# Kernel tuning notes

Measured on AMD Instinct MI355X. Metric: run time of the kernel, lower is better.

The kernel has to match this reference:

```python
import jax, jax.numpy as jnp
import numpy as np

B, SEQ, D = 4, 1024, 1024
H = 16
HD = D // H            # 64, matches cos/sin last dim
S_COLS, TOPK = 8, 2
INTER = 768            # find_multiple(round(1.0 * D * 2 / 3), 256)
EPS = 1e-5


def setup_inputs() -> dict:
    key = jax.random.key(0)
    ks = jax.random.split(key, 6)
    hidden_states = jax.random.normal(ks[0], (B, SEQ, D), jnp.float32)
    # RoPE tables (standard rotary, theta=10000)
    inv_freq = 1.0 / (10000.0 ** (jnp.arange(0, HD, 2, dtype=jnp.float32) / HD))
    freqs = jnp.outer(jnp.arange(SEQ, dtype=jnp.float32), inv_freq)
    emb = jnp.concatenate([freqs, freqs], axis=-1)  # [SEQ, HD]
    cos, sin = jnp.cos(emb), jnp.sin(emb)
    Wr = jax.random.normal(ks[1], (S_COLS, D), jnp.float32) * 0.02
    temperature = jnp.ones((1,), jnp.float32)
    # Stacked per-column TransformerBlock params (bias-free linears)
    Wqkv = jax.random.normal(ks[2], (S_COLS, D, 3 * D), jnp.float32) * 0.02
    Wo = jax.random.normal(ks[3], (S_COLS, D, D), jnp.float32) * 0.02
    Wgu = jax.random.normal(ks[4], (S_COLS, D, 2 * INTER), jnp.float32) * 0.02
    Wd = jax.random.normal(ks[5], (S_COLS, INTER, D), jnp.float32) * 0.02
    return dict(hidden_states=hidden_states, cos=cos, sin=sin, Wr=Wr,
                temperature=temperature, Wqkv=Wqkv, Wo=Wo, Wgu=Wgu, Wd=Wd)


def _rms_norm(x):
    return x * jax.lax.rsqrt(jnp.mean(x * x, axis=-1, keepdims=True) + EPS)


def _rotate_half(x):
    x1, x2 = jnp.split(x, 2, axis=-1)
    return jnp.concatenate([-x2, x1], axis=-1)


def _columns_forward(x, Wqkv, Wo, Wgu, Wd, cos, sin):
    # x: [n, seq, D] dispatched sequences; params gathered per dispatch entry [n, ...]
    n, seq, d = x.shape
    qkv = jnp.einsum('nsd,nde->nse', x, Wqkv)
    q, k, v = jnp.split(qkv, 3, axis=-1)
    q = q.reshape(n, seq, H, HD)
    k = k.reshape(n, seq, H, HD)
    v = v.reshape(n, seq, H, HD)
    c = cos[None, :, None, :]
    s = sin[None, :, None, :]
    q = q * c + _rotate_half(q) * s
    k = k * c + _rotate_half(k) * s
    scores = jnp.einsum('nqhd,nkhd->nhqk', q, k) / jnp.sqrt(jnp.asarray(HD, x.dtype))
    attn = jax.nn.softmax(scores, axis=-1)  # non-causal (HRM-style block)
    ctx = jnp.einsum('nhqk,nkhd->nqhd', attn, v).reshape(n, seq, d)
    attn_out = jnp.einsum('nsd,nde->nse', ctx, Wo)
    x = _rms_norm(x + attn_out)                      # post-norm residual
    gu = jnp.einsum('nsd,nde->nse', x, Wgu)
    gate, up = jnp.split(gu, 2, axis=-1)
    mlp_out = jnp.einsum('nsi,nid->nsd', jax.nn.silu(gate) * up, Wd)
    return _rms_norm(x + mlp_out)


def reference(hidden_states, cos, sin, Wr, temperature, Wqkv, Wo, Wgu, Wd):
    Bn = hidden_states.shape[0]
    temp = jnp.clip(temperature, 0.1, 10.0)
    routing_logits = (hidden_states.mean(axis=1) @ Wr.T) / temp   # [B, S]
    topk_vals, topk_idx = jax.lax.top_k(routing_logits, TOPK)
    weights = jax.nn.softmax(topk_vals, axis=-1)                  # [B, k]
    flat_idx = topk_idx.reshape(-1)                               # [B*k] expert ids
    flat_w = weights.reshape(-1)
    sample_idx = jnp.repeat(jnp.arange(Bn), TOPK)                 # [B*k]
    # Sparse dispatch: exactly B*k block forwards via per-entry param gather
    x_disp = hidden_states[sample_idx]
    col_out = _columns_forward(x_disp, Wqkv[flat_idx], Wo[flat_idx],
                               Wgu[flat_idx], Wd[flat_idx], cos, sin)
    result = jnp.zeros_like(hidden_states).at[sample_idx].add(
        flat_w[:, None, None] * col_out)
    return result, routing_logits
```

## Files before the change

kernel.cpp:

```cpp
#include <hip/hip_runtime.h>
#include <hip/hip_bf16.h>
#include <math.h>

#define B_     4
#define SEQ_   1024
#define D_     1024
#define H_     16
#define NE_    8
#define INTER_ 768
#define EPS_   1e-5f

typedef unsigned short u16;
typedef __attribute__((ext_vector_type(8))) short s8v;
typedef __attribute__((ext_vector_type(4))) short s4v;
typedef __attribute__((ext_vector_type(4))) float f4v;
typedef __attribute__((ext_vector_type(4))) unsigned short u16x4;
typedef __attribute__((ext_vector_type(8))) unsigned short u16x8;

__device__ __forceinline__ u16 f2bf(float x) {
    union { float f; unsigned u; } c; c.f = x;
    unsigned r = (c.u + 0x7FFFu + ((c.u >> 16) & 1u)) >> 16;
    return (u16)r;
}
__device__ __forceinline__ float bf2f(u16 h) {
    union { unsigned u; float f; } c; c.u = ((unsigned)h) << 16;
    return c.f;
}
__device__ __forceinline__ unsigned pk2(float a, float b) {
    union { float f; unsigned u; } x, y; x.f = a; y.f = b;
    return ((x.u + 0x8000u) >> 16) | ((y.u + 0x8000u) & 0xffff0000u);
}

#define GLDS16(gp, lp) \
    __builtin_amdgcn_global_load_lds((const __attribute__((address_space(1))) unsigned int*)(gp), \
                                     (__attribute__((address_space(3))) unsigned int*)(lp), 16, 0, 0)

#define BARRIER()  asm volatile("s_barrier" ::: "memory")

__global__ void route1(const float* __restrict__ hidden, float* __restrict__ part,
                       u16* __restrict__ hb) {
    int b = blockIdx.x, ch = blockIdx.y, t = threadIdx.x;
    const float* xb = hidden + (size_t)b * SEQ_ * D_ + (size_t)ch * 32 * D_;
    u16* ho = hb + (size_t)b * SEQ_ * D_ + (size_t)ch * 32 * D_;
    float4 acc = make_float4(0.f, 0.f, 0.f, 0.f);
    for (int r = 0; r < 32; ++r) {
        float4 v = *(const float4*)&xb[(size_t)r * D_ + t * 4];
        acc.x += v.x; acc.y += v.y; acc.z += v.z; acc.w += v.w;
        u16x4 o = {f2bf(v.x), f2bf(v.y), f2bf(v.z), f2bf(v.w)};
        *(u16x4*)&ho[(size_t)r * D_ + t * 4] = o;
    }
    *(float4*)&part[((size_t)(b * 32 + ch)) * D_ + t * 4] = acc;
}

__global__ void route2(const float* __restrict__ part, const float* __restrict__ Wr,
                       const float* __restrict__ temp, float* __restrict__ out_logits,
                       int* __restrict__ flat_idx, float* __restrict__ flat_w) {
    __shared__ float col[1024];
    __shared__ float sm[8];
    int b = blockIdx.x, t = threadIdx.x;
    float4 s = make_float4(0.f, 0.f, 0.f, 0.f);
    for (int ch = 0; ch < 32; ++ch) {
        float4 v = *(const float4*)&part[((size_t)(b * 32 + ch)) * D_ + t * 4];
        s.x += v.x; s.y += v.y; s.z += v.z; s.w += v.w;
    }
    col[t * 4 + 0] = s.x * (1.f / 1024.f);
    col[t * 4 + 1] = s.y * (1.f / 1024.f);
    col[t * 4 + 2] = s.z * (1.f / 1024.f);
    col[t * 4 + 3] = s.w * (1.f / 1024.f);
    __syncthreads();
    int j = t >> 5, d0 = t & 31;
    float p = 0.f;
    for (int d = d0; d < 1024; d += 32) p += col[d] * Wr[j * 1024 + d];
    for (int off = 16; off >= 1; off >>= 1) p += __shfl_down(p, off, 32);
    if (d0 == 0) sm[j] = p;
    __syncthreads();
    if (t == 0) {
        float tc = temp[0];
        tc = fminf(fmaxf(tc, 0.1f), 10.0f);
        float lg[8];
        for (int jj = 0; jj < 8; ++jj) {
            lg[jj] = sm[jj] / tc;
            out_logits[b * 8 + jj] = lg[jj];
        }
        int i0 = 0; float v0 = lg[0];
        for (int jj = 1; jj < 8; ++jj) if (lg[jj] > v0) { v0 = lg[jj]; i0 = jj; }
        int i1 = -1; float v1 = -1e30f;
        for (int jj = 0; jj < 8; ++jj) if (jj != i0 && lg[jj] > v1) { v1 = lg[jj]; i1 = jj; }
        float e1 = expf(v1 - v0);
        flat_idx[2 * b]     = i0;
        flat_idx[2 * b + 1] = i1;
        flat_w[2 * b]       = 1.0f / (1.0f + e1);
        flat_w[2 * b + 1]   = e1 / (1.0f + e1);
    }
}

__global__ __launch_bounds__(256) void wtrans_all(const float* __restrict__ Wqkv,
                                                  const float* __restrict__ Wo,
                                                  const float* __restrict__ Wgu,
                                                  const float* __restrict__ Wd,
                                                  u16* __restrict__ WqkvT, u16* __restrict__ WoT,
                                                  u16* __restrict__ WguT, u16* __restrict__ WdT,
                                                  const int* __restrict__ flat_idx) {
    int bid = blockIdx.x;
    const float* W; u16* Wt; int K, N, nx, gu = 0;
    if (bid < 6144)      { W = Wqkv; Wt = WqkvT; K = 1024; N = 3072; nx = 48; }
    else if (bid < 8192) { bid -= 6144;  W = Wo;  Wt = WoT;  K = 1024; N = 1024; nx = 16; }
    else if (bid < 11264){ bid -= 8192;  W = Wgu; Wt = WguT; K = 1024; N = 1536; nx = 24; gu = 1; }
    else                 { bid -= 11264; W = Wd;  Wt = WdT;  K = 768;  N = 1024; nx = 16; }
    int x = bid % nx; bid /= nx;
    int ny = K >> 6;
    int y = bid % ny;
    int e = bid / ny;

    bool used = false;
#pragma unroll
    for (int jj = 0; jj < 8; ++jj) used |= (flat_idx[jj] == e);
    if (!used) return;

    __shared__ float tile[64][65];
    int k0 = y * 64, n0 = x * 64;
    const float* Wp = W + (size_t)e * K * N;
    u16* Wtp = Wt + (size_t)e * K * N;
    int t = threadIdx.x;
    int kk = t >> 4, ns = t & 15;
#pragma unroll
    for (int p = 0; p < 4; ++p) {
        float4 v = *(const float4*)&Wp[(size_t)(k0 + kk + p * 16) * N + n0 + ns * 4];
        tile[kk + p * 16][ns * 4 + 0] = v.x;
        tile[kk + p * 16][ns * 4 + 1] = v.y;
        tile[kk + p * 16][ns * 4 + 2] = v.z;
        tile[kk + p * 16][ns * 4 + 3] = v.w;
    }
    __syncthreads();
    int nn = t >> 3, ks = t & 7;
#pragma unroll
    for (int p = 0; p < 2; ++p) {
        int n = n0 + nn + p * 32;
        int nd = n;
        if (gu) nd = (n < 768) ? ((n >> 4) << 5) + (n & 15)
                               : (((n - 768) >> 4) << 5) + 16 + (n & 15);
        u16x8 o;
#pragma unroll
        for (int jj = 0; jj < 8; ++jj) o[jj] = f2bf(tile[ks * 8 + jj][nn + p * 32]);
        *(u16x8*)&Wtp[(size_t)nd * K + k0 + ks * 8] = o;
    }
}

#define GEMM_STAGE(Ap_, Wp_, Kp_, k0v, bo)                                                  \
    {                                                                                       \
        _Pragma("unroll") for (int it = 0; it < 2; ++it) {                                  \
            int p = it * 256 + w * 64 + lane;                                               \
            int row = p >> 2, seg = (p & 3) ^ ((row >> 1) & 3);                             \
            GLDS16((Ap_) + (size_t)(m0 + row) * (Kp_) + (k0v) + seg * 8,                    \
                   As + (bo) + (size_t)(it * 256 + w * 64) * 8);                            \
            GLDS16((Wp_) + (size_t)(n0 + row) * (Kp_) + (k0v) + seg * 8,                    \
                   Bs + (bo) + (size_t)(it * 256 + w * 64) * 8);                            \
        }                                                                                   \
    }

#define GEMM_CORE(Ap_, Wp_, Kp_)                                                            \
    f4v acc[4][4];                                                                          \
    _Pragma("unroll") for (int i = 0; i < 4; ++i)                                           \
        _Pragma("unroll") for (int jj = 0; jj < 4; ++jj) acc[i][jj] = (f4v){0.f,0.f,0.f,0.f}; \
    const int NT = (Kp_) / 32;                                                              \
    GEMM_STAGE(Ap_, Wp_, Kp_, 0, 0)                                                         \
    GEMM_STAGE(Ap_, Wp_, Kp_, 32, 4096)                                                     \
    GEMM_STAGE(Ap_, Wp_, Kp_, 64, 8192)                                                     \
    asm volatile("s_waitcnt vmcnt(8)" ::: "memory");                                        \
    BARRIER();                                                                              \
    int cb = 0;                                                                             \
    for (int kt = 0; kt < NT; ++kt) {                                                       \
        int bo = cb * 4096;                                                                 \
        s8v af[4], bfr[4];                                                                  \
        _Pragma("unroll") for (int ti = 0; ti < 4; ++ti) {                                  \
            int r = wm + ti * 16 + c;                                                       \
            af[ti]  = *(const s8v*)&As[bo + r * 32 + (g ^ ((r >> 1) & 3)) * 8];             \
        }                                                                                   \
        _Pragma("unroll") for (int tj = 0; tj < 4; ++tj) {                                  \
            int r = wn + tj * 16 + c;                                                       \
            bfr[tj] = *(const s8v*)&Bs[bo + r * 32 + (g ^ ((r >> 1) & 3)) * 8];             \
        }                                                                                   \
        __builtin_amdgcn_s_setprio(1);                                                      \
        _Pragma("unroll") for (int ti = 0; ti < 4; ++ti)                                    \
            _Pragma("unroll") for (int tj = 0; tj < 4; ++tj)                                \
                acc[ti][tj] = __builtin_amdgcn_mfma_f32_16x16x32_bf16(af[ti], bfr[tj], acc[ti][tj], 0, 0, 0); \
        __builtin_amdgcn_s_setprio(0);                                                      \
        BARRIER();                                                                          \
        if (kt + 3 < NT) {                                                                  \
            GEMM_STAGE(Ap_, Wp_, Kp_, (kt + 3) * 32, bo)                                    \
            asm volatile("s_waitcnt vmcnt(8)" ::: "memory");                                \
        } else if (kt + 2 < NT) {                                                           \
            asm volatile("s_waitcnt vmcnt(4)" ::: "memory");                                \
        } else {                                                                            \
            asm volatile("s_waitcnt vmcnt(0)" ::: "memory");                                \
        }                                                                                   \
        BARRIER();                                                                          \
        cb = (cb == 2) ? 0 : cb + 1;                                                        \
    }

__global__ __launch_bounds__(256) void gemm_bf16(const u16* __restrict__ Abase,
                                                 const u16* __restrict__ Wtbase,
                                                 u16* __restrict__ Cb,
                                                 const int* __restrict__ flat_idx,
                                                 int M, int N, int K, int aDiv) {
    __shared__ __align__(16) u16 As[3 * 128 * 32];
    __shared__ __align__(16) u16 Bs[3 * 128 * 32];
    int e = blockIdx.z;
    const u16* A  = Abase + (size_t)(e / aDiv) * M * K;
    const u16* Wt = Wtbase + (size_t)flat_idx[e] * N * K;
    int m0 = blockIdx.y * 128, n0 = blockIdx.x * 128;
    int t = threadIdx.x, lane = t & 63, w = t >> 6;
    int g = lane >> 4, c = lane & 15;
    int wm = (w >> 1) * 64, wn = (w & 1) * 64;

    GEMM_CORE(A, Wt, K)

    u16* C = Cb + (size_t)e * M * N;
#pragma unroll
    for (int ti = 0; ti < 4; ++ti)
#pragma unroll
        for (int tj = 0; tj < 4; ++tj)
#pragma unroll
            for (int i = 0; i < 4; ++i)
                C[(size_t)(m0 + wm + ti * 16 + g * 4 + i) * N + n0 + wn + tj * 16 + c] = f2bf(acc[ti][tj][i]);
}

__global__ __launch_bounds__(256) void gemm_qkv(const u16* __restrict__ Abase,
                                                const u16* __restrict__ Wtbase,
                                                const int* __restrict__ flat_idx,
                                                const float* __restrict__ cosb,
                                                const float* __restrict__ sinb,
                                                u16* __restrict__ Qb, u16* __restrict__ Kb,
                                                u16* __restrict__ Vb) {
    __shared__ __align__(16) u16 As[3 * 128 * 32];
    __shared__ __align__(16) u16 Bs[3 * 128 * 32];
    const int K = 1024, N = 3072;
    int e = blockIdx.z;
    const u16* A  = Abase + (size_t)(e >> 1) * 1024 * K;
    const u16* Wt = Wtbase + (size_t)flat_idx[e] * N * K;
    int m0 = blockIdx.y * 128, n0 = blockIdx.x * 128;
    int t = threadIdx.x, lane = t & 63, w = t >> 6;
    int g = lane >> 4, c = lane & 15;
    int wm = (w >> 1) * 64, wn = (w & 1) * 64;

    GEMM_CORE(A, Wt, K)

    int col0 = n0 + wn;
    int sb = m0 + wm + g * 4;
    if (col0 < 2048) {
        bool isq = col0 < 1024;
        u16* dst = isq ? Qb : Kb;
        int h = (col0 & 1023) >> 6;
        const float scl = isq ? 0.125f * 1.44269504f : 1.0f;
#pragma unroll
        for (int ti = 0; ti < 4; ++ti)
#pragma unroll
            for (int i = 0; i < 4; ++i) {
                int s = sb + ti * 16 + i;
                size_t ob = ((size_t)(e * 1024) + s) * 1024 + h * 64;
#pragma unroll
                for (int tj = 0; tj < 2; ++tj) {
                    int d = tj * 16 + c;
                    float x1 = acc[ti][tj][i], x2 = acc[ti][tj + 2][i];
                    float c1 = cosb[s * 64 + d],      s1 = sinb[s * 64 + d];
                    float c2 = cosb[s * 64 + d + 32], s2 = sinb[s * 64 + d + 32];
                    dst[ob + d]      = f2bf((x1 * c1 - x2 * s1) * scl);
                    dst[ob + d + 32] = f2bf((x2 * c2 + x1 * s2) * scl);
                }
            }
    } else {
        int vcol = col0 - 2048;
#pragma unroll
        for (int ti = 0; ti < 4; ++ti)
#pragma unroll
            for (int tj = 0; tj < 4; ++tj)
#pragma unroll
                for (int i = 0; i < 4; ++i)
                    Vb[((size_t)(e * 1024) + sb + ti * 16 + i) * 1024 + vcol + tj * 16 + c] = f2bf(acc[ti][tj][i]);
    }
}

__global__ __launch_bounds__(256) void gemm_wgu_silu(const u16* __restrict__ Abase,
                                                     const u16* __restrict__ Wtbase,
                                                     u16* __restrict__ act,
                                                     const int* __restrict__ flat_idx) {
    __shared__ __align__(16) u16 As[3 * 128 * 32];
    __shared__ __align__(16) u16 Bs[3 * 128 * 32];
    const int K = 1024, N = 1536;
    int e = blockIdx.z;
    const u16* A  = Abase + (size_t)e * 1024 * K;
    const u16* Wt = Wtbase + (size_t)flat_idx[e] * N * K;
    int m0 = blockIdx.y * 128, n0 = blockIdx.x * 128;
    int t = threadIdx.x, lane = t & 63, w = t >> 6;
    int g = lane >> 4, c = lane & 15;
    int wm = (w >> 1) * 64, wn = (w & 1) * 64;

    GEMM_CORE(A, Wt, K)

    int col0 = n0 + wn;
    int oc0 = (col0 >> 1) + c;
    int sb = m0 + wm + g * 4;
#pragma unroll
    for (int ti = 0; ti < 4; ++ti)
#pragma unroll
        for (int i = 0; i < 4; ++i) {
            size_t rb = ((size_t)(e * 1024) + sb + ti * 16 + i) * 768;
#pragma unroll
            for (int pr = 0; pr < 2; ++pr) {
                float gt = acc[ti][pr * 2][i];
                float up = acc[ti][pr * 2 + 1][i];
                act[rb + oc0 + pr * 16] = f2bf(gt / (1.f + __expf(-gt)) * up);
            }
        }
}

__global__ __launch_bounds__(256) void vtrans(const u16* __restrict__ Vb, u16* __restrict__ Vtg) {
    __shared__ __align__(16) u16 tile[64 * 72];
    int s0 = blockIdx.x * 64;
    int eh = blockIdx.y;
    int e = eh >> 4, h = eh & 15;
    int t = threadIdx.x;
#pragma unroll
    for (int it = 0; it < 2; ++it) {
        int p = it * 256 + t;
        int sr = p >> 3, ds = p & 7;
        u16x8 v = *(const u16x8*)&Vb[((size_t)(e * 1024) + s0 + sr) * 1024 + h * 64 + ds * 8];
        *(u16x8*)&tile[sr * 72 + ds * 8] = v;
    }
    __syncthreads();
#pragma unroll
    for (int it = 0; it < 2; ++it) {
        int p = it * 256 + t;
        int d = p >> 3, ks = p & 7;
        u16x8 o;
#pragma unroll
        for (int jj = 0; jj < 8; ++jj) o[jj] = tile[(ks * 8 + jj) * 72 + d];
        *(u16x8*)&Vtg[((size_t)((e * 16 + h) * 64) + d) * 1024 + s0 + ks * 8] = o;
    }
}

#define ATTN_STAGE(ktv, bo)                                                                 \
    {                                                                                       \
        _Pragma("unroll") for (int it = 0; it < 2; ++it) {                                  \
            int p = it * 256 + w * 64 + lane;                                               \
            int row = p >> 3, ss = p & 7;                                                   \
            GLDS16(Kb + ((size_t)(e * 1024 + (ktv) * 64 + row)) * 1024 + h * 64 + (ss ^ (row & 7)) * 8, \
                   Ks + (bo) + (size_t)(it * 256 + w * 64) * 8);                            \
            GLDS16(Vtg + ((size_t)((e * 16 + h) * 64 + row)) * 1024 + (ktv) * 64 + (ss ^ (row & 7)) * 8, \
                   Vt + (bo) + (size_t)(it * 256 + w * 64) * 8);                            \
        }                                                                                   \
    }

__global__ __launch_bounds__(256) void attn_mfma(const u16* __restrict__ Qb, const u16* __restrict__ Kb,
                                                 const u16* __restrict__ Vtg, u16* __restrict__ ctx) {
    __shared__ __align__(16) u16 Ks[2 * 64 * 64];
    __shared__ __align__(16) u16 Vt[2 * 64 * 64];
    int e = blockIdx.x, h = blockIdx.y, qt = blockIdx.z;
    int t = threadIdx.x, lane = t & 63, w = t >> 6;
    int g = lane >> 4, c = lane & 15;
    int q0 = qt * 64 + w * 16;

    s8v qf[2];
#pragma unroll
    for (int ks = 0; ks < 2; ++ks)
        qf[ks] = *(const s8v*)&Qb[((size_t)(e * 1024) + q0 + c) * 1024 + h * 64 + ks * 32 + g * 8];

    f4v O[4];
#pragma unroll
    for (int tj = 0; tj < 4; ++tj) O[tj] = (f4v){0.f, 0.f, 0.f, 0.f};
    f4v liacc = (f4v){0.f, 0.f, 0.f, 0.f};
    const s4v vone = {(short)0x3F80, (short)0x3F80, (short)0x3F80, (short)0x3F80};

    ATTN_STAGE(0, 0)
    ATTN_STAGE(1, 4096)
    asm volatile("s_waitcnt vmcnt(4)" ::: "memory");
    BARRIER();
    int cb = 0;

    for (int kt = 0; kt < 16; ++kt) {
        int bo = cb * 4096;
        f4v st[4];
#pragma unroll
        for (int tj = 0; tj < 4; ++tj) st[tj] = (f4v){0.f, 0.f, 0.f, 0.f};
#pragma unroll
        for (int ks = 0; ks < 2; ++ks)
#pragma unroll
            for (int tj = 0; tj < 4; ++tj) {
                int kvl = tj * 16 + c;
                s8v kf = *(const s8v*)&Ks[bo + kvl * 64 + (((ks * 4 + g) ^ (kvl & 7)) * 8)];
                st[tj] = __builtin_amdgcn_mfma_f32_16x16x32_bf16(kf, qf[ks], st[tj], 0, 0, 0);
            }

        s4v pf[4];
#pragma unroll
        for (int tj = 0; tj < 4; ++tj) {
            float p0 = __builtin_amdgcn_exp2f(st[tj][0]);
            float p1 = __builtin_amdgcn_exp2f(st[tj][1]);
            float p2 = __builtin_amdgcn_exp2f(st[tj][2]);
            float p3 = __builtin_amdgcn_exp2f(st[tj][3]);
            union { unsigned u[2]; s4v v; } pu;
            pu.u[0] = pk2(p0, p1);
            pu.u[1] = pk2(p2, p3);
            pf[tj] = pu.v;
        }

#pragma unroll
        for (int tjC = 0; tjC < 4; ++tjC) {
            liacc = __builtin_amdgcn_mfma_f32_16x16x16bf16_1k(pf[tjC], vone, liacc, 0, 0, 0);
#pragma unroll
            for (int tjd = 0; tjd < 4; ++tjd) {
                int d = tjd * 16 + c;
                int sd = tjC * 2 + (g >> 1);
                s4v vf = *(const s4v*)&Vt[bo + d * 64 + ((sd ^ (d & 7)) * 8) + (g & 1) * 4];
                O[tjd] = __builtin_amdgcn_mfma_f32_16x16x16bf16_1k(pf[tjC], vf, O[tjd], 0, 0, 0);
            }
        }

        BARRIER();
        if (kt + 2 < 16) {
            ATTN_STAGE(kt + 2, bo)
            asm volatile("s_waitcnt vmcnt(4)" ::: "memory");
        } else {
            asm volatile("s_waitcnt vmcnt(0)" ::: "memory");
        }
        BARRIER();
        cb ^= 1;
    }
#pragma unroll
    for (int i = 0; i < 4; ++i) {
        float linv = 1.0f / liacc[i];
        size_t rbase = ((size_t)(e * 1024) + q0 + g * 4 + i) * 1024 + h * 64;
#pragma unroll
        for (int tjd = 0; tjd < 4; ++tjd)
            ctx[rbase + tjd * 16 + c] = f2bf(O[tjd][i] * linv);
    }
}

__global__ void add_rmsnorm(const u16* __restrict__ hb, const u16* __restrict__ aob,
                            u16* __restrict__ xnb) {
    int row = blockIdx.x;
    int e = row >> 10;
    int b = e >> 1;
    int s = row & 1023;
    const u16* xr = hb + (((size_t)b * SEQ_ + s) << 10);
    const u16* ar = aob + ((size_t)row << 10);
    u16* o = xnb + ((size_t)row << 10);
    int t = threadIdx.x;
    u16x4 xv = *(const u16x4*)&xr[t * 4];
    u16x4 av = *(const u16x4*)&ar[t * 4];
    float v[4];
    float ss = 0.f;
#pragma unroll
    for (int i = 0; i < 4; ++i) {
        v[i] = bf2f(xv[i]) + bf2f(av[i]);
        ss += v[i] * v[i];
    }
    for (int off = 32; off >= 1; off >>= 1) ss += __shfl_down(ss, off, 64);
    __shared__ float wred[4];
    if ((t & 63) == 0) wred[t >> 6] = ss;
    __syncthreads();
    float tot = wred[0] + wred[1] + wred[2] + wred[3];
    float scale = rsqrtf(tot * (1.0f / 1024.0f) + EPS_);
    u16x4 ov;
#pragma unroll
    for (int i = 0; i < 4; ++i) ov[i] = f2bf(v[i] * scale);
    *(u16x4*)&o[t * 4] = ov;
}

__global__ void final_kernel(const u16* __restrict__ xnb, const u16* __restrict__ mlpb,
                             const float* __restrict__ flat_w, float* __restrict__ out) {
    int row = blockIdx.x;
    int b = row >> 10;
    int s = row & 1023;
    int t = threadIdx.x;
    __shared__ float wred[4];
    float res[4] = {0.f, 0.f, 0.f, 0.f};
    for (int j = 0; j < 2; ++j) {
        int e = 2 * b + j;
        size_t off = (((size_t)e * SEQ_ + s) << 10);
        u16x4 xv = *(const u16x4*)&xnb[off + t * 4];
        u16x4 mv = *(const u16x4*)&mlpb[off + t * 4];
        float v[4];
        float ss = 0.f;
#pragma unroll
        for (int i = 0; i < 4; ++i) {
            v[i] = bf2f(xv[i]) + bf2f(mv[i]);
            ss += v[i] * v[i];
        }
        for (int off2 = 32; off2 >= 1; off2 >>= 1) ss += __shfl_down(ss, off2, 64);
        if ((t & 63) == 0) wred[t >> 6] = ss;
        __syncthreads();
        float tot = wred[0] + wred[1] + wred[2] + wred[3];
        float scale = rsqrtf(tot * (1.0f / 1024.0f) + EPS_);
        float wgt = flat_w[e];
#pragma unroll
        for (int i = 0; i < 4; ++i) res[i] += wgt * v[i] * scale;
        __syncthreads();
    }
    float* o = out + ((size_t)row << 10);
    *(float4*)&o[t * 4] = make_float4(res[0], res[1], res[2], res[3]);
}

extern "C" void kernel_launch(void* const* d_in, const int* in_sizes, int n_in,
                              void* d_out, int out_size, void* d_ws, size_t ws_size,
                              hipStream_t stream) {
    const float* hidden = (const float*)d_in[0];
    const float* cosb   = (const float*)d_in[1];
    const float* sinb   = (const float*)d_in[2];
    const float* Wr     = (const float*)d_in[3];
    const float* temp   = (const float*)d_in[4];
    const float* Wqkv   = (const float*)d_in[5];
    const float* Wo     = (const float*)d_in[6];
    const float* Wgu    = (const float*)d_in[7];
    const float* Wd     = (const float*)d_in[8];
    float* out = (float*)d_out;
    float* out_logits = out + (size_t)B_ * SEQ_ * D_;

    char* base = (char*)d_ws;
    int*   flat_idx = (int*)base;
    float* flat_w   = (float*)(base + 128);
    float* routeP   = (float*)(base + 4096);
    size_t off = (size_t)1 << 20;
    u16* WqkvT = (u16*)(base + off); off += (size_t)8 * 3072 * 1024 * 2;
    u16* WoT   = (u16*)(base + off); off += (size_t)8 * 1024 * 1024 * 2;
    u16* WguT  = (u16*)(base + off); off += (size_t)8 * 1536 * 1024 * 2;
    u16* WdT   = (u16*)(base + off); off += (size_t)8 * 1024 * 768 * 2;
    u16* hb    = (u16*)(base + off); off += (size_t)4 * 1024 * 1024 * 2;
    u16* Qb    = (u16*)(base + off); off += (size_t)8 * 1024 * 1024 * 2;
    u16* Kb    = (u16*)(base + off); off += (size_t)8 * 1024 * 1024 * 2;
    u16* Vb    = (u16*)(base + off); off += (size_t)8 * 1024 * 1024 * 2;
    u16* Vtg   = (u16*)(base + off); off += (size_t)8 * 1024 * 1024 * 2;
    u16* ctxb  = (u16*)(base + off); off += (size_t)8 * 1024 * 1024 * 2;
    u16* aob   = (u16*)(base + off); off += (size_t)8 * 1024 * 1024 * 2;
    u16* xnb   = (u16*)(base + off); off += (size_t)8 * 1024 * 1024 * 2;
    u16* actb  = (u16*)(base + off); off += (size_t)8 * 1024 * 768 * 2;
    u16* mlpb  = (u16*)(base + off); off += (size_t)8 * 1024 * 1024 * 2;

    route1<<<dim3(4, 32), 256, 0, stream>>>(hidden, routeP, hb);
    route2<<<4, 256, 0, stream>>>(routeP, Wr, temp, out_logits, flat_idx, flat_w);
    wtrans_all<<<12800, 256, 0, stream>>>(Wqkv, Wo, Wgu, Wd, WqkvT, WoT, WguT, WdT, flat_idx);

    gemm_qkv<<<dim3(24, 8, 8), 256, 0, stream>>>(hb, WqkvT, flat_idx, cosb, sinb, Qb, Kb, Vb);
    vtrans<<<dim3(16, 128), 256, 0, stream>>>(Vb, Vtg);
    attn_mfma<<<dim3(8, 16, 16), 256, 0, stream>>>(Qb, Kb, Vtg, ctxb);
    gemm_bf16<<<dim3(8, 8, 8), 256, 0, stream>>>(ctxb, WoT, aob, flat_idx, 1024, 1024, 1024, 1);
    add_rmsnorm<<<NE_ * SEQ_, 256, 0, stream>>>(hb, aob, xnb);
    gemm_wgu_silu<<<dim3(12, 8, 8), 256, 0, stream>>>(xnb, WguT, actb, flat_idx);
    gemm_bf16<<<dim3(8, 8, 8), 256, 0, stream>>>(actb, WdT, mlpb, flat_idx, 1024, 1024, 768, 1);
    final_kernel<<<B_ * SEQ_, 256, 0, stream>>>(xnb, mlpb, flat_w, out);
}
```

Baseline: 523.2 us.

## Use single-buffered K=64 GEMM tiles and process 128 query rows per attention block

Replaces the triple-buffered K=32 GEMM pipeline with a simpler single-buffered K=64 loop, using precomputed swizzled global pointers and two barriers per step. The attention kernel now has each warp handle two 16-row query sub-tiles, so every K/V tile staged in LDS is reused across 128 queries and the grid is halved. The GEMM change loses the load/compute overlap of the old pipeline but uses less LDS per block, which could allow more resident blocks. The attention change raises register pressure.

```diff
diff --git a/kernel.cpp b/kernel.cpp
--- a/kernel.cpp
+++ b/kernel.cpp
@@ -146,56 +146,41 @@
     }
 }
 
-#define GEMM_STAGE(Ap_, Wp_, Kp_, k0v, bo)                                                  \
-    {                                                                                       \
-        _Pragma("unroll") for (int it = 0; it < 2; ++it) {                                  \
-            int p = it * 256 + w * 64 + lane;                                               \
-            int row = p >> 2, seg = (p & 3) ^ ((row >> 1) & 3);                             \
-            GLDS16((Ap_) + (size_t)(m0 + row) * (Kp_) + (k0v) + seg * 8,                    \
-                   As + (bo) + (size_t)(it * 256 + w * 64) * 8);                            \
-            GLDS16((Wp_) + (size_t)(n0 + row) * (Kp_) + (k0v) + seg * 8,                    \
-                   Bs + (bo) + (size_t)(it * 256 + w * 64) * 8);                            \
+#define GEMM_CORE64(Ap_, Wp_, Kp_)                                                          \
+    f4v acc[4][4];                                                                          \
+    _Pragma("unroll") for (int i_ = 0; i_ < 4; ++i_)                                        \
+        _Pragma("unroll") for (int j_ = 0; j_ < 4; ++j_) acc[i_][j_] = (f4v){0.f,0.f,0.f,0.f}; \
+    const u16* gA[4]; const u16* gB[4];                                                     \
+    _Pragma("unroll") for (int it = 0; it < 4; ++it) {                                      \
+        int p_ = it * 256 + t;                                                              \
+        int row_ = p_ >> 3, seg_ = (p_ & 7) ^ (row_ & 7);                                   \
+        gA[it] = (Ap_) + (size_t)(m0 + row_) * (Kp_) + seg_ * 8;                            \
+        gB[it] = (Wp_) + (size_t)(n0 + row_) * (Kp_) + seg_ * 8;                            \
+    }                                                                                       \
+    const int NT = (Kp_) / 64;                                                              \
+    for (int kt = 0; kt < NT; ++kt) {                                                       \
+        _Pragma("unroll") for (int it = 0; it < 4; ++it) {                                  \
+            GLDS16(gA[it] + (size_t)kt * 64, As + (size_t)(it * 256 + w * 64) * 8);         \
+            GLDS16(gB[it] + (size_t)kt * 64, Bs + (size_t)(it * 256 + w * 64) * 8);         \
         }                                                                                   \
-    }
-
-#define GEMM_CORE(Ap_, Wp_, Kp_)                                                            \
-    f4v acc[4][4];                                                                          \
-    _Pragma("unroll") for (int i = 0; i < 4; ++i)                                           \
-        _Pragma("unroll") for (int jj = 0; jj < 4; ++jj) acc[i][jj] = (f4v){0.f,0.f,0.f,0.f}; \
-    const int NT = (Kp_) / 32;                                                              \
-    GEMM_STAGE(Ap_, Wp_, Kp_, 0, 0)                                                         \
-    GEMM_STAGE(Ap_, Wp_, Kp_, 32, 4096)                                                     \
-    GEMM_STAGE(Ap_, Wp_, Kp_, 64, 8192)                                                     \
-    asm volatile("s_waitcnt vmcnt(8)" ::: "memory");                                        \
-    BARRIER();                                                                              \
-    int cb = 0;                                                                             \
-    for (int kt = 0; kt < NT; ++kt) {                                                       \
-        int bo = cb * 4096;                                                                 \
-        s8v af[4], bfr[4];                                                                  \
-        _Pragma("unroll") for (int ti = 0; ti < 4; ++ti) {                                  \
-            int r = wm + ti * 16 + c;                                                       \
-            af[ti]  = *(const s8v*)&As[bo + r * 32 + (g ^ ((r >> 1) & 3)) * 8];             \
+        __syncthreads();                                                                    \
+        _Pragma("unroll") for (int ks = 0; ks < 2; ++ks) {                                  \
+            s8v af[4], bfr[4];                                                              \
+            _Pragma("unroll") for (int ti = 0; ti < 4; ++ti) {                              \
+                int r = wm + ti * 16 + c;                                                   \
+                af[ti]  = *(const s8v*)&As[r * 64 + (((ks * 4 + g) ^ (r & 7)) * 8)];        \
+            }                                                                               \
+            _Pragma("unroll") for (int tj = 0; tj < 4; ++tj) {                              \
+                int r = wn + tj * 16 + c;                                                   \
+                bfr[tj] = *(const s8v*)&Bs[r * 64 + (((ks * 4 + g) ^ (r & 7)) * 8)];        \
+            }                                                                               \
+            __builtin_amdgcn_s_setprio(1);                                                  \
+            _Pragma("unroll") for (int ti = 0; ti < 4; ++ti)                                \
+                _Pragma("unroll") for (int tj = 0; tj < 4; ++tj)                            \
+                    acc[ti][tj] = __builtin_amdgcn_mfma_f32_16x16x32_bf16(af[ti], bfr[tj], acc[ti][tj], 0, 0, 0); \
+            __builtin_amdgcn_s_setprio(0);                                                  \
         }                                                                                   \
-        _Pragma("unroll") for (int tj = 0; tj < 4; ++tj) {                                  \
-            int r = wn + tj * 16 + c;                                                       \
-            bfr[tj] = *(const s8v*)&Bs[bo + r * 32 + (g ^ ((r >> 1) & 3)) * 8];             \
-        }                                                                                   \
-        __builtin_amdgcn_s_setprio(1);                                                      \
-        _Pragma("unroll") for (int ti = 0; ti < 4; ++ti)                                    \
-            _Pragma("unroll") for (int tj = 0; tj < 4; ++tj)                                \
-                acc[ti][tj] = __builtin_amdgcn_mfma_f32_16x16x32_bf16(af[ti], bfr[tj], acc[ti][tj], 0, 0, 0); \
-        __builtin_amdgcn_s_setprio(0);                                                      \
-        BARRIER();                                                                          \
-        if (kt + 3 < NT) {                                                                  \
-            GEMM_STAGE(Ap_, Wp_, Kp_, (kt + 3) * 32, bo)                                    \
-            asm volatile("s_waitcnt vmcnt(8)" ::: "memory");                                \
-        } else if (kt + 2 < NT) {                                                           \
-            asm volatile("s_waitcnt vmcnt(4)" ::: "memory");                                \
-        } else {                                                                            \
-            asm volatile("s_waitcnt vmcnt(0)" ::: "memory");                                \
-        }                                                                                   \
-        BARRIER();                                                                          \
-        cb = (cb == 2) ? 0 : cb + 1;                                                        \
+        __syncthreads();                                                                    \
     }
 
 __global__ __launch_bounds__(256) void gemm_bf16(const u16* __restrict__ Abase,
@@ -203,8 +188,8 @@
                                                  u16* __restrict__ Cb,
                                                  const int* __restrict__ flat_idx,
                                                  int M, int N, int K, int aDiv) {
-    __shared__ __align__(16) u16 As[3 * 128 * 32];
-    __shared__ __align__(16) u16 Bs[3 * 128 * 32];
+    __shared__ __align__(16) u16 As[128 * 64];
+    __shared__ __align__(16) u16 Bs[128 * 64];
     int e = blockIdx.z;
     const u16* A  = Abase + (size_t)(e / aDiv) * M * K;
     const u16* Wt = Wtbase + (size_t)flat_idx[e] * N * K;
@@ -213,7 +198,7 @@
     int g = lane >> 4, c = lane & 15;
     int wm = (w >> 1) * 64, wn = (w & 1) * 64;
 
-    GEMM_CORE(A, Wt, K)
+    GEMM_CORE64(A, Wt, K)
 
     u16* C = Cb + (size_t)e * M * N;
 #pragma unroll
@@ -232,8 +217,8 @@
                                                 const float* __restrict__ sinb,
                                                 u16* __restrict__ Qb, u16* __restrict__ Kb,
                                                 u16* __restrict__ Vb) {
-    __shared__ __align__(16) u16 As[3 * 128 * 32];
-    __shared__ __align__(16) u16 Bs[3 * 128 * 32];
+    __shared__ __align__(16) u16 As[128 * 64];
+    __shared__ __align__(16) u16 Bs[128 * 64];
     const int K = 1024, N = 3072;
     int e = blockIdx.z;
     const u16* A  = Abase + (size_t)(e >> 1) * 1024 * K;
@@ -243,7 +228,7 @@
     int g = lane >> 4, c = lane & 15;
     int wm = (w >> 1) * 64, wn = (w & 1) * 64;
 
-    GEMM_CORE(A, Wt, K)
+    GEMM_CORE64(A, Wt, K)
 
     int col0 = n0 + wn;
     int sb = m0 + wm + g * 4;
@@ -284,8 +269,8 @@
                                                      const u16* __restrict__ Wtbase,
                                                      u16* __restrict__ act,
                                                      const int* __restrict__ flat_idx) {
-    __shared__ __align__(16) u16 As[3 * 128 * 32];
-    __shared__ __align__(16) u16 Bs[3 * 128 * 32];
+    __shared__ __align__(16) u16 As[128 * 64];
+    __shared__ __align__(16) u16 Bs[128 * 64];
     const int K = 1024, N = 1536;
     int e = blockIdx.z;
     const u16* A  = Abase + (size_t)e * 1024 * K;
@@ -295,7 +280,7 @@
     int g = lane >> 4, c = lane & 15;
     int wm = (w >> 1) * 64, wn = (w & 1) * 64;
 
-    GEMM_CORE(A, Wt, K)
+    GEMM_CORE64(A, Wt, K)
 
     int col0 = n0 + wn;
     int oc0 = (col0 >> 1) + c;
@@ -342,12 +327,8 @@
 #define ATTN_STAGE(ktv, bo)                                                                 \
     {                                                                                       \
         _Pragma("unroll") for (int it = 0; it < 2; ++it) {                                  \
-            int p = it * 256 + w * 64 + lane;                                               \
-            int row = p >> 3, ss = p & 7;                                                   \
-            GLDS16(Kb + ((size_t)(e * 1024 + (ktv) * 64 + row)) * 1024 + h * 64 + (ss ^ (row & 7)) * 8, \
-                   Ks + (bo) + (size_t)(it * 256 + w * 64) * 8);                            \
-            GLDS16(Vtg + ((size_t)((e * 16 + h) * 64 + row)) * 1024 + (ktv) * 64 + (ss ^ (row & 7)) * 8, \
-                   Vt + (bo) + (size_t)(it * 256 + w * 64) * 8);                            \
+            GLDS16(gK[it] + (size_t)(ktv) * 64 * 1024, Ks + (bo) + (size_t)(it * 256 + w * 64) * 8); \
+            GLDS16(gV[it] + (size_t)(ktv) * 64,        Vt + (bo) + (size_t)(it * 256 + w * 64) * 8); \
         }                                                                                   \
     }
 
@@ -358,18 +339,33 @@
     int e = blockIdx.x, h = blockIdx.y, qt = blockIdx.z;
     int t = threadIdx.x, lane = t & 63, w = t >> 6;
     int g = lane >> 4, c = lane & 15;
-    int q0 = qt * 64 + w * 16;
-
-    s8v qf[2];
-#pragma unroll
-    for (int ks = 0; ks < 2; ++ks)
-        qf[ks] = *(const s8v*)&Qb[((size_t)(e * 1024) + q0 + c) * 1024 + h * 64 + ks * 32 + g * 8];
-
-    f4v O[4];
-#pragma unroll
-    for (int tj = 0; tj < 4; ++tj) O[tj] = (f4v){0.f, 0.f, 0.f, 0.f};
-    f4v liacc = (f4v){0.f, 0.f, 0.f, 0.f};
+    int q0 = qt * 128 + w * 16;
+
+    s8v qf[2][2];
+#pragma unroll
+    for (int qs = 0; qs < 2; ++qs)
+#pragma unroll
+        for (int ks = 0; ks < 2; ++ks)
+            qf[qs][ks] = *(const s8v*)&Qb[((size_t)(e * 1024) + q0 + qs * 64 + c) * 1024 + h * 64 + ks * 32 + g * 8];
+
+    f4v O[2][4];
+    f4v li[2];
+#pragma unroll
+    for (int qs = 0; qs < 2; ++qs) {
+        li[qs] = (f4v){0.f, 0.f, 0.f, 0.f};
+#pragma unroll
+        for (int tj = 0; tj < 4; ++tj) O[qs][tj] = (f4v){0.f, 0.f, 0.f, 0.f};
+    }
     const s4v vone = {(short)0x3F80, (short)0x3F80, (short)0x3F80, (short)0x3F80};
+
+    const u16* gK[2]; const u16* gV[2];
+#pragma unroll
+    for (int it = 0; it < 2; ++it) {
+        int p = it * 256 + t;
+        int row = p >> 3, ss = p & 7;
+        gK[it] = Kb + ((size_t)(e * 1024 + row)) * 1024 + h * 64 + ((ss ^ (row & 7)) * 8);
+        gV[it] = Vtg + ((size_t)((e * 16 + h) * 64 + row)) * 1024 + ((ss ^ (row & 7)) * 8);
+    }
 
     ATTN_STAGE(0, 0)
     ATTN_STAGE(1, 4096)
@@ -379,40 +375,43 @@
 
     for (int kt = 0; kt < 16; ++kt) {
         int bo = cb * 4096;
-        f4v st[4];
-#pragma unroll
-        for (int tj = 0; tj < 4; ++tj) st[tj] = (f4v){0.f, 0.f, 0.f, 0.f};
-#pragma unroll
-        for (int ks = 0; ks < 2; ++ks)
+#pragma unroll
+        for (int qs = 0; qs < 2; ++qs) {
+            f4v st[4];
+#pragma unroll
+            for (int tj = 0; tj < 4; ++tj) st[tj] = (f4v){0.f, 0.f, 0.f, 0.f};
+#pragma unroll
+            for (int ks = 0; ks < 2; ++ks)
+#pragma unroll
+                for (int tj = 0; tj < 4; ++tj) {
+                    int kvl = tj * 16 + c;
+                    s8v kf = *(const s8v*)&Ks[bo + kvl * 64 + (((ks * 4 + g) ^ (kvl & 7)) * 8)];
+                    st[tj] = __builtin_amdgcn_mfma_f32_16x16x32_bf16(kf, qf[qs][ks], st[tj], 0, 0, 0);
+                }
+
+            s4v pf[4];
 #pragma unroll
             for (int tj = 0; tj < 4; ++tj) {
-                int kvl = tj * 16 + c;
-                s8v kf = *(const s8v*)&Ks[bo + kvl * 64 + (((ks * 4 + g) ^ (kvl & 7)) * 8)];
-                st[tj] = __builtin_amdgcn_mfma_f32_16x16x32_bf16(kf, qf[ks], st[tj], 0, 0, 0);
+                float p0 = __builtin_amdgcn_exp2f(st[tj][0]);
+                float p1 = __builtin_amdgcn_exp2f(st[tj][1]);
+                float p2 = __builtin_amdgcn_exp2f(st[tj][2]);
+                float p3 = __builtin_amdgcn_exp2f(st[tj][3]);
+                union { unsigned u[2]; s4v v; } pu;
+                pu.u[0] = pk2(p0, p1);
+                pu.u[1] = pk2(p2, p3);
+                pf[tj] = pu.v;
             }
 
-        s4v pf[4];
-#pragma unroll
-        for (int tj = 0; tj < 4; ++tj) {
-            float p0 = __builtin_amdgcn_exp2f(st[tj][0]);
-            float p1 = __builtin_amdgcn_exp2f(st[tj][1]);
-            float p2 = __builtin_amdgcn_exp2f(st[tj][2]);
-            float p3 = __builtin_amdgcn_exp2f(st[tj][3]);
-            union { unsigned u[2]; s4v v; } pu;
-            pu.u[0] = pk2(p0, p1);
-            pu.u[1] = pk2(p2, p3);
-            pf[tj] = pu.v;
-        }
-
-#pragma unroll
-        for (int tjC = 0; tjC < 4; ++tjC) {
-            liacc = __builtin_amdgcn_mfma_f32_16x16x16bf16_1k(pf[tjC], vone, liacc, 0, 0, 0);
-#pragma unroll
-            for (int tjd = 0; tjd < 4; ++tjd) {
-                int d = tjd * 16 + c;
-                int sd = tjC * 2 + (g >> 1);
-                s4v vf = *(const s4v*)&Vt[bo + d * 64 + ((sd ^ (d & 7)) * 8) + (g & 1) * 4];
-                O[tjd] = __builtin_amdgcn_mfma_f32_16x16x16bf16_1k(pf[tjC], vf, O[tjd], 0, 0, 0);
+#pragma unroll
+            for (int tjC = 0; tjC < 4; ++tjC) {
+                li[qs] = __builtin_amdgcn_mfma_f32_16x16x16bf16_1k(pf[tjC], vone, li[qs], 0, 0, 0);
+#pragma unroll
+                for (int tjd = 0; tjd < 4; ++tjd) {
+                    int d = tjd * 16 + c;
+                    int sd = tjC * 2 + (g >> 1);
+                    s4v vf = *(const s4v*)&Vt[bo + d * 64 + ((sd ^ (d & 7)) * 8) + (g & 1) * 4];
+                    O[qs][tjd] = __builtin_amdgcn_mfma_f32_16x16x16bf16_1k(pf[tjC], vf, O[qs][tjd], 0, 0, 0);
+                }
             }
         }
 
@@ -427,13 +426,15 @@
         cb ^= 1;
     }
 #pragma unroll
-    for (int i = 0; i < 4; ++i) {
-        float linv = 1.0f / liacc[i];
-        size_t rbase = ((size_t)(e * 1024) + q0 + g * 4 + i) * 1024 + h * 64;
-#pragma unroll
-        for (int tjd = 0; tjd < 4; ++tjd)
-            ctx[rbase + tjd * 16 + c] = f2bf(O[tjd][i] * linv);
-    }
+    for (int qs = 0; qs < 2; ++qs)
+#pragma unroll
+        for (int i = 0; i < 4; ++i) {
+            float linv = 1.0f / li[qs][i];
+            size_t rbase = ((size_t)(e * 1024) + q0 + qs * 64 + g * 4 + i) * 1024 + h * 64;
+#pragma unroll
+            for (int tjd = 0; tjd < 4; ++tjd)
+                ctx[rbase + tjd * 16 + c] = f2bf(O[qs][tjd][i] * linv);
+        }
 }
 
 __global__ void add_rmsnorm(const u16* __restrict__ hb, const u16* __restrict__ aob,
@@ -542,7 +543,7 @@
 
     gemm_qkv<<<dim3(24, 8, 8), 256, 0, stream>>>(hb, WqkvT, flat_idx, cosb, sinb, Qb, Kb, Vb);
     vtrans<<<dim3(16, 128), 256, 0, stream>>>(Vb, Vtg);
-    attn_mfma<<<dim3(8, 16, 16), 256, 0, stream>>>(Qb, Kb, Vtg, ctxb);
+    attn_mfma<<<dim3(8, 16, 8), 256, 0, stream>>>(Qb, Kb, Vtg, ctxb);
     gemm_bf16<<<dim3(8, 8, 8), 256, 0, stream>>>(ctxb, WoT, aob, flat_idx, 1024, 1024, 1024, 1);
     add_rmsnorm<<<NE_ * SEQ_, 256, 0, stream>>>(hb, aob, xnb);
     gemm_wgu_silu<<<dim3(12, 8, 8), 256, 0, stream>>>(xnb, WguT, actb, flat_idx);
```

Measured after the change: 486.3 us, median of 2. -7.1%, faster.
